# Optimization experiments

Measured on AMD Instinct MI355X. Metric: run time of the kernel, lower is better.

Reference implementation:

```python
import jax, jax.numpy as jnp
import numpy as np
import math

B, Q, H, KVH, D, KV, HID = 2, 1024, 32, 8, 128, 4096, 4096

def rotate_half(x):
    x1, x2 = jnp.split(x, 2, axis=-1)
    return jnp.concatenate([-x2, x1], axis=-1)

def setup_inputs() -> dict:
    key = jax.random.key(0)
    ks = jax.random.split(key, 10)
    inv = 1.0 / math.sqrt(HID)
    return {
        "hidden_states": jax.random.normal(ks[0], (B, Q, HID), dtype=jnp.float32),
        "cos": jax.random.uniform(ks[1], (B, 1, Q, D), dtype=jnp.float32),
        "sin": jax.random.uniform(ks[2], (B, 1, Q, D), dtype=jnp.float32),
        "attention_mask": jnp.zeros((B, 1, Q, KV), dtype=jnp.float32),
        "cache_k": jax.random.normal(ks[3], (B, KVH, KV, D), dtype=jnp.float32),
        "cache_v": jax.random.normal(ks[4], (B, KVH, KV, D), dtype=jnp.float32),
        "sink_ids": jnp.arange(Q, dtype=jnp.int32),
        "Wq": jax.random.normal(ks[5], (H * D, HID), dtype=jnp.float32) * inv,
        "Wk": jax.random.normal(ks[6], (KVH * D, HID), dtype=jnp.float32) * inv,
        "Wv": jax.random.normal(ks[7], (KVH * D, HID), dtype=jnp.float32) * inv,
        "Wo": jax.random.normal(ks[8], (HID, H * D), dtype=jnp.float32) * inv,
    }

def reference(hidden_states, cos, sin, attention_mask, cache_k, cache_v, sink_ids, Wq, Wk, Wv, Wo):
    b, q_len, hid = hidden_states.shape
    d = cos.shape[-1]
    h = Wq.shape[0] // d
    kvh = Wk.shape[0] // d
    n_rep = h // kvh

    # projections -> (b, heads, q, d)
    qs = (hidden_states @ Wq.T).reshape(b, q_len, h, d).transpose(0, 2, 1, 3)
    ks = (hidden_states @ Wk.T).reshape(b, q_len, kvh, d).transpose(0, 2, 1, 3)
    vs = (hidden_states @ Wv.T).reshape(b, q_len, kvh, d).transpose(0, 2, 1, 3)

    # RoPE
    qs = qs * cos + rotate_half(qs) * sin
    ks = ks * cos + rotate_half(ks) * sin

    # sink new K/V into the paged cache at sink_ids, then read back the full cache
    k_cache = cache_k.at[:, :, sink_ids, :].set(ks)
    v_cache = cache_v.at[:, :, sink_ids, :].set(vs)

    # repeat_kv: (b, kvh, kv, d) -> (b, h, kv, d)
    k_full = jnp.repeat(k_cache, n_rep, axis=1)
    v_full = jnp.repeat(v_cache, n_rep, axis=1)

    scores = jnp.einsum('bhqd,bhkd->bhqk', qs, k_full) / math.sqrt(d)
    scores = scores + attention_mask
    attn = jax.nn.softmax(scores.astype(jnp.float32), axis=-1).astype(qs.dtype)
    out = jnp.einsum('bhqk,bhkd->bhqd', attn, v_full)
    out = out.transpose(0, 2, 1, 3).reshape(b, q_len, h * d)
    return out @ Wo.T
```

## Files before the change

### kernel.cpp

```cpp
#include <hip/hip_runtime.h>

typedef __bf16 bf16;
typedef __attribute__((ext_vector_type(8))) __bf16 bf16x8;
typedef __attribute__((ext_vector_type(4))) __bf16 bf16x4;
typedef __attribute__((ext_vector_type(4))) float floatx4;

#define LOG2E 1.4426950408889634f
#define CEXP (0.08838834764831845f * 1.4426950408889634f)

__device__ __forceinline__ void lds16(const void* g, void* l) {
  __builtin_amdgcn_global_load_lds(
      (const __attribute__((address_space(1))) unsigned int*)(unsigned long long)g,
      (__attribute__((address_space(3))) unsigned int*)(unsigned int)(unsigned long long)l,
      16, 0, 0);
}

template <typename CT>
__global__ __launch_bounds__(256) void gemm_bt(const bf16* __restrict__ A,
                                               const bf16* __restrict__ W,
                                               CT* __restrict__ C,
                                               int M, int N, int K) {
  __shared__ bf16 sA[128 * 32];
  __shared__ bf16 sB[128 * 32];
  const int tid = threadIdx.x;
  const int lane = tid & 63;
  const int wave = tid >> 6;
  const int quad = lane >> 4;
  const int l16 = lane & 15;
  const int m0 = blockIdx.y * 128;
  const int n0 = blockIdx.x * 128;
  const int wm = (wave >> 1) * 64;
  const int wn = (wave & 1) * 64;

  floatx4 acc[4][4] = {};

  const int srow = tid >> 2;
  const int cs = tid & 3;
  const int clog = cs ^ ((srow >> 1) & 3);
  const bf16* gA = A + (long)(m0 + srow) * K + clog * 8;
  const bf16* gB = W + (long)(n0 + srow) * K + clog * 8;
  bf16* lA = sA + wave * 512;
  bf16* lB = sB + wave * 512;
  const long step64 = (long)64 * K;
  const int cq = quad ^ ((l16 >> 1) & 3);

  for (int k0 = 0; k0 < K; k0 += 32) {
    lds16(gA, lA);
    lds16(gA + step64, lA + 2048);
    lds16(gB, lB);
    lds16(gB + step64, lB + 2048);
    gA += 32;
    gB += 32;
    __syncthreads();
    bf16x8 af[4], bfr[4];
#pragma unroll
    for (int i = 0; i < 4; ++i)
      af[i] = *(const bf16x8*)(sA + (wm + i * 16 + l16) * 32 + cq * 8);
#pragma unroll
    for (int j = 0; j < 4; ++j)
      bfr[j] = *(const bf16x8*)(sB + (wn + j * 16 + l16) * 32 + cq * 8);
#pragma unroll
    for (int i = 0; i < 4; ++i)
#pragma unroll
      for (int j = 0; j < 4; ++j)
        acc[i][j] = __builtin_amdgcn_mfma_f32_16x16x32_bf16(af[i], bfr[j], acc[i][j], 0, 0, 0);
    __syncthreads();
  }

#pragma unroll
  for (int i = 0; i < 4; ++i) {
    const int row = m0 + wm + i * 16 + quad * 4;
#pragma unroll
    for (int j = 0; j < 4; ++j) {
      const int col = n0 + wn + j * 16 + l16;
#pragma unroll
      for (int r = 0; r < 4; ++r)
        C[(long)(row + r) * N + col] = (CT)acc[i][j][r];
    }
  }
}

__global__ __launch_bounds__(256, 2) void attn(const bf16* __restrict__ qr,
                                               const bf16* __restrict__ kc,
                                               const bf16* __restrict__ vt,
                                               const float* __restrict__ mask,
                                               const int* __restrict__ flag,
                                               bf16* __restrict__ o) {
  __shared__ bf16 sK[2][64 * 128];
  __shared__ bf16 sV[2][128 * 64];
  __shared__ bf16 sP[4 * 32 * 64];
  const int tid = threadIdx.x, lane = tid & 63, wave = tid >> 6;
  const int quad = lane >> 4, l16 = lane & 15;

  int id = blockIdx.x;
  const int kvh = id & 7;
  id >>= 3;
  const int b = id & 1;
  id >>= 1;
  const int h = kvh * 4 + (id & 3);
  const int q0 = (id >> 2) * 128;
  const int qw = q0 + wave * 32;

  const bf16* qbase = qr + ((long)(b * 32 + h) * 1024 + qw) * 128;
  bf16x8 qf[2][4];
#pragma unroll
  for (int qt = 0; qt < 2; ++qt)
#pragma unroll
    for (int ks = 0; ks < 4; ++ks)
      qf[qt][ks] = *(const bf16x8*)(qbase + (long)(qt * 16 + l16) * 128 +
                                    ks * 32 + quad * 8);

  floatx4 oacc[8][2] = {};
  floatx4 lrun4[2] = {};

  const bool use_mask = (*flag != 0);
  const bf16* kbase = kc + (long)(b * 8 + kvh) * 4096 * 128;
  const bf16* vbase = vt + (long)(b * 8 + kvh) * 128 * 4096;
  bf16* sPw = sP + wave * 2048;

  auto stage = [&](int buf, int kt) {
    const int kv0 = kt * 64;
#pragma unroll
    for (int it = 0; it < 4; ++it) {
      const int r0 = wave * 16 + it * 4;
      const int row = r0 + (lane >> 4);
      lds16(kbase + (long)(kv0 + row) * 128 + (((lane & 15) ^ (row & 15)) << 3),
            sK[buf] + r0 * 128);
    }
#pragma unroll
    for (int it = 0; it < 4; ++it) {
      const int r0 = wave * 32 + it * 8;
      const int row = r0 + (lane >> 3);
      lds16(vbase + (long)row * 4096 + kv0 + (((lane & 7) ^ (row & 7)) << 3),
            sV[buf] + r0 * 64);
    }
  };

  stage(0, 0);
  __syncthreads();

  for (int kt = 0; kt < 64; ++kt) {
    const int cur = kt & 1;
    const int kv0 = kt * 64;
    if (kt < 63) stage(cur ^ 1, kt + 1);

    floatx4 s[4][2] = {};
    __builtin_amdgcn_s_setprio(1);
#pragma unroll
    for (int ks = 0; ks < 4; ++ks)
#pragma unroll
      for (int j = 0; j < 4; ++j) {
        const bf16x8 kf = *(const bf16x8*)(sK[cur] + (j * 16 + l16) * 128 +
                                           (((ks * 4 + quad) ^ l16) << 3));
        s[j][0] = __builtin_amdgcn_mfma_f32_16x16x32_bf16(kf, qf[0][ks], s[j][0], 0, 0, 0);
        s[j][1] = __builtin_amdgcn_mfma_f32_16x16x32_bf16(kf, qf[1][ks], s[j][1], 0, 0, 0);
      }
    __builtin_amdgcn_s_setprio(0);

    if (use_mask) {
#pragma unroll
      for (int qt = 0; qt < 2; ++qt)
#pragma unroll
        for (int j = 0; j < 4; ++j)
#pragma unroll
          for (int r = 0; r < 4; ++r) {
            const int q = qw + qt * 16 + l16;
            const int kv = kv0 + j * 16 + quad * 4 + r;
            s[j][qt][r] += mask[((long)b * 1024 + q) * 4096 + kv] * LOG2E;
          }
    }

#pragma unroll
    for (int qt = 0; qt < 2; ++qt)
#pragma unroll
      for (int j = 0; j < 4; ++j) {
        bf16x4 pk;
        floatx4 pv;
#pragma unroll
        for (int r = 0; r < 4; ++r) {
          pv[r] = exp2f(s[j][qt][r]);
          pk[r] = (bf16)pv[r];
        }
        lrun4[qt] += pv;
        *(bf16x4*)(sPw + (qt * 16 + l16) * 64 +
                   (((j * 2 + (quad >> 1)) ^ (l16 & 7)) << 3) + ((quad & 1) << 2)) = pk;
      }

    __builtin_amdgcn_s_setprio(1);
#pragma unroll
    for (int kc2 = 0; kc2 < 2; ++kc2) {
      const int ph = ((kc2 * 4 + quad) ^ (l16 & 7)) << 3;
      const bf16x8 pf0 = *(const bf16x8*)(sPw + l16 * 64 + ph);
      const bf16x8 pf1 = *(const bf16x8*)(sPw + (16 + l16) * 64 + ph);
#pragma unroll
      for (int mt = 0; mt < 8; ++mt) {
        const bf16x8 vf = *(const bf16x8*)(sV[cur] + (mt * 16 + l16) * 64 + ph);
        oacc[mt][0] = __builtin_amdgcn_mfma_f32_16x16x32_bf16(vf, pf0, oacc[mt][0], 0, 0, 0);
        oacc[mt][1] = __builtin_amdgcn_mfma_f32_16x16x32_bf16(vf, pf1, oacc[mt][1], 0, 0, 0);
      }
    }
    __builtin_amdgcn_s_setprio(0);

    __syncthreads();
  }

#pragma unroll
  for (int qt = 0; qt < 2; ++qt) {
    float ls = (lrun4[qt][0] + lrun4[qt][1]) + (lrun4[qt][2] + lrun4[qt][3]);
    ls += __shfl_xor(ls, 16, 64);
    ls += __shfl_xor(ls, 32, 64);
    const float inv = 1.f / ls;
    const int q = qw + qt * 16 + l16;
    bf16* op = o + ((long)(b * 1024 + q) * 32 + h) * 128 + quad * 4;
#pragma unroll
    for (int mt = 0; mt < 8; ++mt) {
      bf16x4 ov;
#pragma unroll
      for (int r = 0; r < 4; ++r) ov[r] = (bf16)(oacc[mt][qt][r] * inv);
      *(bf16x4*)(op + mt * 16) = ov;
    }
  }
}

__global__ void zeroflag(int* f) { *f = 0; }

__global__ void prep(const floatx4* __restrict__ hid, const floatx4* __restrict__ wq,
                     const floatx4* __restrict__ wk, const floatx4* __restrict__ wv,
                     const floatx4* __restrict__ ck, const floatx4* __restrict__ mask,
                     bf16x4* __restrict__ hidb, bf16x4* __restrict__ wqkvb,
                     bf16x4* __restrict__ kcb, int* __restrict__ flag) {
  const int bid = blockIdx.x;
  const int tid = threadIdx.x;
  if (bid >= 40960) {
    const long i = (long)(bid - 40960) * 256 + tid;
    const floatx4 v = mask[i];
    if (v[0] != 0.f || v[1] != 0.f || v[2] != 0.f || v[3] != 0.f) atomicOr(flag, 1);
    return;
  }
  const floatx4* in;
  bf16x4* out;
  long i;
  if (bid < 8192)       { i = (long)bid * 256 + tid;           in = hid; out = hidb; }
  else if (bid < 24576) { i = (long)(bid - 8192) * 256 + tid;  in = wq;  out = wqkvb; }
  else if (bid < 28672) { i = (long)(bid - 24576) * 256 + tid; in = wk;  out = wqkvb + 4194304; }
  else if (bid < 32768) { i = (long)(bid - 28672) * 256 + tid; in = wv;  out = wqkvb + 5242880; }
  else                  { i = (long)(bid - 32768) * 256 + tid; in = ck;  out = kcb; }
  const floatx4 v = in[i];
  bf16x4 o;
  o[0] = (bf16)v[0]; o[1] = (bf16)v[1]; o[2] = (bf16)v[2]; o[3] = (bf16)v[3];
  out[i] = o;
}

__global__ void f2b4(const floatx4* __restrict__ in, bf16x4* __restrict__ out) {
  const long i = (long)blockIdx.x * 256 + threadIdx.x;
  const floatx4 v = in[i];
  bf16x4 o;
  o[0] = (bf16)v[0]; o[1] = (bf16)v[1]; o[2] = (bf16)v[2]; o[3] = (bf16)v[3];
  out[i] = o;
}

__global__ void vtrans(const float* __restrict__ v, bf16* __restrict__ vt) {
  __shared__ float t[64][33];
  const int bk = blockIdx.z;
  const int kv0 = blockIdx.x * 64, d0 = blockIdx.y * 32;
  const int tid = threadIdx.x;
  const float* src = v + ((long)bk * 4096 + kv0) * 128 + d0;
  const int rr = tid >> 5, cc = tid & 31;
#pragma unroll
  for (int p = 0; p < 8; ++p)
    t[p * 8 + rr][cc] = src[(long)(p * 8 + rr) * 128 + cc];
  __syncthreads();
  const int rowD = tid >> 3, oct = tid & 7;
  bf16x8 o;
#pragma unroll
  for (int i = 0; i < 8; ++i) o[i] = (bf16)t[oct * 8 + i][rowD];
  *(bf16x8*)(vt + ((long)bk * 128 + d0 + rowD) * 4096 + kv0 + oct * 8) = o;
}

__global__ void ropes(const bf16* __restrict__ qkv, const float* __restrict__ cosp,
                      const float* __restrict__ sinp, const int* __restrict__ sink,
                      bf16* __restrict__ qrope, bf16* __restrict__ kcb,
                      bf16* __restrict__ vtb) {
  const int bid = blockIdx.x;
  const int tid = threadIdx.x;
  if (bid < 4096) {
    const int t = bid * 256 + tid;
    const int j = t & 15;
    const int q = (t >> 4) & 1023;
    const int h = (t >> 14) & 31;
    const int b = t >> 19;
    const long qrow = ((long)b * 1024 + q) * 6144 + h * 128;
    const bf16x4 x = *(const bf16x4*)(qkv + qrow + j * 4);
    const bf16x4 y = *(const bf16x4*)(qkv + qrow + 64 + j * 4);
    const long ci = ((long)b * 1024 + q) * 128 + j * 4;
    const floatx4 cl = *(const floatx4*)(cosp + ci);
    const floatx4 sl = *(const floatx4*)(sinp + ci);
    const floatx4 ch = *(const floatx4*)(cosp + ci + 64);
    const floatx4 sh = *(const floatx4*)(sinp + ci + 64);
    bf16x4 xo, yo;
#pragma unroll
    for (int i = 0; i < 4; ++i) {
      const float xf = (float)x[i], yf = (float)y[i];
      xo[i] = (bf16)((xf * cl[i] - yf * sl[i]) * CEXP);
      yo[i] = (bf16)((yf * ch[i] + xf * sh[i]) * CEXP);
    }
    bf16* ob = qrope + ((long)(b * 32 + h) * 1024 + q) * 128 + j * 4;
    *(bf16x4*)ob = xo;
    *(bf16x4*)(ob + 64) = yo;
  } else if (bid < 5120) {
    const int t = (bid - 4096) * 256 + tid;
    const int j = t & 15;
    const int q = (t >> 4) & 1023;
    const int kvh = (t >> 14) & 7;
    const int b = t >> 17;
    const long krow = ((long)b * 1024 + q) * 6144 + 4096 + kvh * 128;
    const bf16x4 x = *(const bf16x4*)(qkv + krow + j * 4);
    const bf16x4 y = *(const bf16x4*)(qkv + krow + 64 + j * 4);
    const long ci = ((long)b * 1024 + q) * 128 + j * 4;
    const floatx4 cl = *(const floatx4*)(cosp + ci);
    const floatx4 sl = *(const floatx4*)(sinp + ci);
    const floatx4 ch = *(const floatx4*)(cosp + ci + 64);
    const floatx4 sh = *(const floatx4*)(sinp + ci + 64);
    bf16x4 xo, yo;
#pragma unroll
    for (int i = 0; i < 4; ++i) {
      const float xf = (float)x[i], yf = (float)y[i];
      xo[i] = (bf16)(xf * cl[i] - yf * sl[i]);
      yo[i] = (bf16)(yf * ch[i] + xf * sh[i]);
    }
    const int sk = sink[q];
    bf16* ob = kcb + (((long)b * 8 + kvh) * 4096 + sk) * 128 + j * 4;
    *(bf16x4*)ob = xo;
    *(bf16x4*)(ob + 64) = yo;
  } else {
    const int t = (bid - 5120) * 256 + tid;
    const int j = t & 15;
    const int q = (t >> 4) & 1023;
    const int kvh = (t >> 14) & 7;
    const int b = t >> 17;
    const bf16x8 v = *(const bf16x8*)(qkv + ((long)b * 1024 + q) * 6144 + 5120 +
                                      kvh * 128 + j * 8);
    const int sk = sink[q];
    bf16* dst = vtb + (((long)b * 8 + kvh) * 128 + j * 8) * 4096 + sk;
#pragma unroll
    for (int i = 0; i < 8; ++i) dst[(long)i * 4096] = v[i];
  }
}

extern "C" void kernel_launch(void* const* d_in, const int* in_sizes, int n_in,
                              void* d_out, int out_size, void* d_ws, size_t ws_size,
                              hipStream_t stream) {
  const float* hid  = (const float*)d_in[0];
  const float* cosp = (const float*)d_in[1];
  const float* sinp = (const float*)d_in[2];
  const float* mask = (const float*)d_in[3];
  const float* ck   = (const float*)d_in[4];
  const float* cv   = (const float*)d_in[5];
  const int*   sink = (const int*)d_in[6];
  const float* Wq   = (const float*)d_in[7];
  const float* Wk   = (const float*)d_in[8];
  const float* Wv   = (const float*)d_in[9];
  const float* Wo   = (const float*)d_in[10];
  float* out = (float*)d_out;

  char* ws = (char*)d_ws;
  bf16* wqkv  = (bf16*)(ws);
  bf16* hidb  = (bf16*)(ws + 50331648);
  bf16* qkvb  = (bf16*)(ws + 67108864);
  bf16* qrope = (bf16*)(ws + 92274688);
  bf16* kcb   = (bf16*)(ws + 109051904);
  bf16* vtb   = (bf16*)(ws + 125829120);
  bf16* ob    = (bf16*)(ws + 142606336);
  int*  flag  = (int*)(ws + 159383552);
  bf16* wob   = (bf16*)(ws + 50331648);

  zeroflag<<<1, 1, 0, stream>>>(flag);

  prep<<<49152, 256, 0, stream>>>((const floatx4*)hid, (const floatx4*)Wq,
                                  (const floatx4*)Wk, (const floatx4*)Wv,
                                  (const floatx4*)ck, (const floatx4*)mask,
                                  (bf16x4*)hidb, (bf16x4*)wqkv, (bf16x4*)kcb, flag);

  vtrans<<<dim3(64, 4, 16), 256, 0, stream>>>(cv, vtb);

  gemm_bt<bf16><<<dim3(48, 16), 256, 0, stream>>>(hidb, wqkv, qkvb, 2048, 6144, 4096);

  ropes<<<6144, 256, 0, stream>>>(qkvb, cosp, sinp, sink, qrope, kcb, vtb);

  f2b4<<<16384, 256, 0, stream>>>((const floatx4*)Wo, (bf16x4*)wob);

  attn<<<512, 256, 0, stream>>>(qrope, kcb, vtb, mask, flag, ob);

  gemm_bt<float><<<dim3(32, 16), 256, 0, stream>>>(ob, wob, out, 2048, 4096, 4096);

  (void)in_sizes; (void)n_in; (void)out_size; (void)ws_size;
}
```

Before: 683.1 us.

## Double-buffer GEMM LDS tiles with BK=64 and async prefetch pipeline

Rewrites the projection GEMM main loop to use two LDS buffers with a K-tile of 64 instead of a single 32-wide buffer. The next tile is issued via global_load_lds while the current one is consumed, using vmcnt waits and raw barriers in place of full syncthreads. The XOR swizzle is widened to 8 chunks to match the wider tile. LDS use per block quadruples (64KB) while launch bounds now request 2 blocks per CU, so occupancy may be limited by LDS.

```diff
diff --git a/kernel.cpp b/kernel.cpp
--- a/kernel.cpp
+++ b/kernel.cpp
@@ -15,13 +15,15 @@
       16, 0, 0);
 }
 
+__device__ __forceinline__ void memfence() { asm volatile("" ::: "memory"); }
+
 template <typename CT>
-__global__ __launch_bounds__(256) void gemm_bt(const bf16* __restrict__ A,
-                                               const bf16* __restrict__ W,
-                                               CT* __restrict__ C,
-                                               int M, int N, int K) {
-  __shared__ bf16 sA[128 * 32];
-  __shared__ bf16 sB[128 * 32];
+__global__ __launch_bounds__(256, 2) void gemm_bt(const bf16* __restrict__ A,
+                                                  const bf16* __restrict__ W,
+                                                  CT* __restrict__ C,
+                                                  int M, int N, int K) {
+  __shared__ bf16 sA[2][128 * 64];
+  __shared__ bf16 sB[2][128 * 64];
   const int tid = threadIdx.x;
   const int lane = tid & 63;
   const int wave = tid >> 6;
@@ -34,37 +36,73 @@
 
   floatx4 acc[4][4] = {};
 
-  const int srow = tid >> 2;
-  const int cs = tid & 3;
-  const int clog = cs ^ ((srow >> 1) & 3);
-  const bf16* gA = A + (long)(m0 + srow) * K + clog * 8;
-  const bf16* gB = W + (long)(n0 + srow) * K + clog * 8;
-  bf16* lA = sA + wave * 512;
-  bf16* lB = sB + wave * 512;
-  const long step64 = (long)64 * K;
-  const int cq = quad ^ ((l16 >> 1) & 3);
-
-  for (int k0 = 0; k0 < K; k0 += 32) {
-    lds16(gA, lA);
-    lds16(gA + step64, lA + 2048);
-    lds16(gB, lB);
-    lds16(gB + step64, lB + 2048);
-    gA += 32;
-    gB += 32;
-    __syncthreads();
-    bf16x8 af[4], bfr[4];
-#pragma unroll
-    for (int i = 0; i < 4; ++i)
-      af[i] = *(const bf16x8*)(sA + (wm + i * 16 + l16) * 32 + cq * 8);
-#pragma unroll
-    for (int j = 0; j < 4; ++j)
-      bfr[j] = *(const bf16x8*)(sB + (wn + j * 16 + l16) * 32 + cq * 8);
-#pragma unroll
-    for (int i = 0; i < 4; ++i)
+  const int rsub = lane >> 3;
+  const int csw = ((lane & 7) ^ rsub) * 8;
+  const int NT = K >> 6;
+
+  auto stage = [&](int buf, int t) {
+    const int k0 = t << 6;
+#pragma unroll
+    for (int i = 0; i < 4; ++i) {
+      const int row = i * 32 + wave * 8 + rsub;
+      lds16(A + (long)(m0 + row) * K + k0 + csw, sA[buf] + (i * 32 + wave * 8) * 64);
+      lds16(W + (long)(n0 + row) * K + k0 + csw, sB[buf] + (i * 32 + wave * 8) * 64);
+    }
+  };
+
+  stage(0, 0);
+  stage(1, 1);
+
+  for (int t = 0; t < NT - 1; ++t) {
+    const int buf = t & 1;
+    asm volatile("s_waitcnt vmcnt(8)" ::: "memory");
+    __builtin_amdgcn_s_barrier();
+    memfence();
+#pragma unroll
+    for (int s = 0; s < 2; ++s) {
+      bf16x8 af[4], bfr[4];
+#pragma unroll
+      for (int i = 0; i < 4; ++i)
+        af[i] = *(const bf16x8*)(sA[buf] + (wm + i * 16 + l16) * 64 +
+                                 (((s * 4 + quad) ^ (l16 & 7)) << 3));
 #pragma unroll
       for (int j = 0; j < 4; ++j)
-        acc[i][j] = __builtin_amdgcn_mfma_f32_16x16x32_bf16(af[i], bfr[j], acc[i][j], 0, 0, 0);
-    __syncthreads();
+        bfr[j] = *(const bf16x8*)(sB[buf] + (wn + j * 16 + l16) * 64 +
+                                  (((s * 4 + quad) ^ (l16 & 7)) << 3));
+#pragma unroll
+      for (int i = 0; i < 4; ++i)
+#pragma unroll
+        for (int j = 0; j < 4; ++j)
+          acc[i][j] = __builtin_amdgcn_mfma_f32_16x16x32_bf16(af[i], bfr[j], acc[i][j], 0, 0, 0);
+    }
+    memfence();
+    __builtin_amdgcn_s_barrier();
+    memfence();
+    if (t + 2 < NT) stage(buf, t + 2);
+  }
+
+  asm volatile("s_waitcnt vmcnt(0)" ::: "memory");
+  __builtin_amdgcn_s_barrier();
+  memfence();
+  {
+    const int buf = (NT - 1) & 1;
+#pragma unroll
+    for (int s = 0; s < 2; ++s) {
+      bf16x8 af[4], bfr[4];
+#pragma unroll
+      for (int i = 0; i < 4; ++i)
+        af[i] = *(const bf16x8*)(sA[buf] + (wm + i * 16 + l16) * 64 +
+                                 (((s * 4 + quad) ^ (l16 & 7)) << 3));
+#pragma unroll
+      for (int j = 0; j < 4; ++j)
+        bfr[j] = *(const bf16x8*)(sB[buf] + (wn + j * 16 + l16) * 64 +
+                                  (((s * 4 + quad) ^ (l16 & 7)) << 3));
+#pragma unroll
+      for (int i = 0; i < 4; ++i)
+#pragma unroll
+        for (int j = 0; j < 4; ++j)
+          acc[i][j] = __builtin_amdgcn_mfma_f32_16x16x32_bf16(af[i], bfr[j], acc[i][j], 0, 0, 0);
+    }
   }
 
 #pragma unroll
```

New measurement: 629.2 us. 7.9% less time.
